# Kernel optimization log

Measured on AMD Instinct MI355X. Metric: run time of the kernel, lower is better.

## Reference

```python
import jax, jax.numpy as jnp
import numpy as np

EMB, HEADS, DEPTH, SEQ, BATCH = 256, 8, 4, 8192, 4
DH = EMB // HEADS  # 32
FF = 4 * EMB
EPS = 1e-5


def setup_inputs() -> dict:
    key = jax.random.key(0)
    ks = jax.random.split(key, 8)
    w = lambda k, shape: jax.random.normal(k, shape, dtype=jnp.float32) * 0.02
    D = DEPTH
    return {
        "x": jax.random.normal(ks[0], (BATCH, SEQ, EMB), dtype=jnp.float32),
        "Wq": w(ks[1], (D, EMB, EMB)),
        "Wk": w(ks[2], (D, EMB, EMB)),
        "Wv": w(ks[3], (D, EMB, EMB)),
        "Wo": w(ks[4], (D, EMB, EMB)),
        "bo": jnp.zeros((D, EMB), jnp.float32),
        "ln1_g": jnp.ones((D, EMB), jnp.float32),
        "ln1_b": jnp.zeros((D, EMB), jnp.float32),
        "W1": w(ks[5], (D, EMB, FF)),
        "b1": jnp.zeros((D, FF), jnp.float32),
        "W2": w(ks[6], (D, FF, EMB)),
        "b2": jnp.zeros((D, EMB), jnp.float32),
        "ln2_g": jnp.ones((D, EMB), jnp.float32),
        "ln2_b": jnp.zeros((D, EMB), jnp.float32),
    }


def _layernorm(x, g, b):
    mu = x.mean(-1, keepdims=True)
    var = ((x - mu) ** 2).mean(-1, keepdims=True)
    return (x - mu) * jax.lax.rsqrt(var + EPS) * g + b


def _linear_attn(x, Wq, Wk, Wv, Wo, bo):
    # lucidrains linear_attn: q,k scaled by d**-0.25; softmax q over feature dim,
    # k over sequence dim; context = k^T v (per head), out = q @ context.
    b, n, dm = x.shape
    split = lambda t: t.reshape(b, n, HEADS, DH).transpose(0, 2, 1, 3)  # -> bhnd
    scale = DH ** -0.25
    q = jax.nn.softmax(split(x @ Wq) * scale, axis=-1)   # over d
    k = jax.nn.softmax(split(x @ Wk) * scale, axis=-2)   # over n
    v = split(x @ Wv)
    context = jnp.einsum('bhnd,bhne->bhde', k, v)        # [b,h,d,d]
    out = jnp.einsum('bhnd,bhde->bhne', q, context)      # [b,h,n,d]
    out = out.transpose(0, 2, 1, 3).reshape(b, n, dm)
    return out @ Wo + bo


def _forward(x, Wq, Wk, Wv, Wo, bo, ln1_g, ln1_b, W1, b1, W2, b2, ln2_g, ln2_b):
    for i in range(DEPTH):
        h = _layernorm(x, ln1_g[i], ln1_b[i])
        x = x + _linear_attn(h, Wq[i], Wk[i], Wv[i], Wo[i], bo[i])
        h = _layernorm(x, ln2_g[i], ln2_b[i])
        x = x + (jax.nn.gelu(h @ W1[i] + b1[i], approximate=False) @ W2[i] + b2[i])
    return x


def reference(x, Wq, Wk, Wv, Wo, bo, ln1_g, ln1_b, W1, b1, W2, b2, ln2_g, ln2_b):
    return _forward(x, Wq, Wk, Wv, Wo, bo, ln1_g, ln1_b, W1, b1, W2, b2, ln2_g, ln2_b)
```

## Files before the change

### kernel.cpp

```cpp
#include <hip/hip_runtime.h>
#include <hip/hip_bf16.h>

typedef __attribute__((ext_vector_type(8))) short bf16x8;
typedef __attribute__((ext_vector_type(4))) float f32x4;

#define EMB 256
#define HEADS 8
#define DH 32
#define SEQ 8192
#define BATCH 4
#define NROWS (SEQ*BATCH)
#define FFD 1024
#define DEPTH 4
#define QKVN 768
#define SCALE 0.42044820762685725f
#define NCHUNK 128
#define ROWS_PER_CHUNK (SEQ/NCHUNK)

static __device__ __forceinline__ float bf2f(ushort u){
  union { unsigned int i; float f; } x; x.i = ((unsigned int)u) << 16; return x.f;
}
static __device__ __forceinline__ ushort f2bf(float f){
  union { __hip_bfloat16 h; ushort u; } cv;
  cv.h = __float2bfloat16(f);
  return cv.u;
}
static __device__ __forceinline__ float gelu_f(float v){
  float y = 0.7978845608028654f * (v + 0.044715f*v*v*v);
  float e = __expf(2.0f*y);
  return 0.5f*v*(1.0f + (1.0f - 2.0f/(e + 1.0f)));
}

static __device__ __forceinline__ void gload_lds16(const ushort* g, ushort* l){
  __builtin_amdgcn_global_load_lds(
      (const __attribute__((address_space(1))) unsigned int*)(uintptr_t)g,
      (__attribute__((address_space(3))) unsigned int*)(uintptr_t)l,
      16, 0, 0);
}

__global__ __launch_bounds__(256) void prep_weights(
    const float* __restrict__ Wq, const float* __restrict__ Wk,
    const float* __restrict__ Wv, const float* __restrict__ Wo,
    const float* __restrict__ W1, const float* __restrict__ W2,
    ushort* __restrict__ wqkv_t, ushort* __restrict__ wo_t,
    ushort* __restrict__ w1_t, ushort* __restrict__ w2_t)
{
  __shared__ float tile[32][33];
  int bid = blockIdx.x;
  int L = bid / 768, r = bid % 768;
  const float* src; ushort* dst; int K, N, tidx;
  if (r < 192){ int which = r >> 6; tidx = r & 63;
    src = (which==0?Wq:which==1?Wk:Wv) + (long)L*65536;
    dst = wqkv_t + (long)L*QKVN*EMB + which*EMB*EMB; K=256; N=256;
  } else if (r < 256){ tidx = r-192; src = Wo + (long)L*65536; dst = wo_t + (long)L*65536; K=256; N=256; }
  else if (r < 512){ tidx = r-256; src = W1 + (long)L*262144; dst = w1_t + (long)L*262144; K=256; N=1024; }
  else { tidx = r-512; src = W2 + (long)L*262144; dst = w2_t + (long)L*262144; K=1024; N=256; }
  int tn = N >> 5;
  int tk = tidx / tn, tj = tidx % tn;
  int k0 = tk*32, n0 = tj*32;
  int c = threadIdx.x & 31, r0 = threadIdx.x >> 5;
  #pragma unroll
  for (int i=0;i<4;i++){
    int rr = r0 + i*8;
    tile[rr][c] = src[(long)(k0+rr)*N + n0 + c];
  }
  __syncthreads();
  #pragma unroll
  for (int i=0;i<4;i++){
    int rr = r0 + i*8;
    dst[(long)(n0+rr)*K + k0 + c] = f2bf(tile[c][rr]);
  }
}

__global__ __launch_bounds__(256) void ln_kernel(const float* __restrict__ x,
    const float* __restrict__ g, const float* __restrict__ bb,
    ushort* __restrict__ h)
{
  int wid = threadIdx.x >> 6, lane = threadIdx.x & 63;
  long row = (long)blockIdx.x*4 + wid;
  const float4 xv = *(const float4*)(x + row*EMB + lane*4);
  float s = xv.x+xv.y+xv.z+xv.w;
  float s2 = xv.x*xv.x+xv.y*xv.y+xv.z*xv.z+xv.w*xv.w;
  #pragma unroll
  for (int m=1;m<64;m<<=1){ s += __shfl_xor(s,m,64); s2 += __shfl_xor(s2,m,64); }
  float mean = s * (1.0f/EMB);
  float inv = rsqrtf(s2*(1.0f/EMB) - mean*mean + 1e-5f);
  float4 gv = *(const float4*)(g + lane*4);
  float4 bv = *(const float4*)(bb + lane*4);
  ushort4 o;
  o.x = f2bf((xv.x-mean)*inv*gv.x + bv.x);
  o.y = f2bf((xv.y-mean)*inv*gv.y + bv.y);
  o.z = f2bf((xv.z-mean)*inv*gv.z + bv.z);
  o.w = f2bf((xv.w-mean)*inv*gv.w + bv.w);
  *(ushort4*)(h + row*EMB + lane*4) = o;
}

template<int MODE, int BM, int BN, int BK, int GSWAP>
__global__ __launch_bounds__(512, 2) void gemm_bt(
    const ushort* __restrict__ A, const ushort* __restrict__ Bt,
    int M, int N, int K,
    const float* __restrict__ bias,
    const float* __restrict__ xinf, const ushort* __restrict__ xinb,
    float* __restrict__ xoutf, ushort* __restrict__ xoutb,
    ushort* __restrict__ outb,
    const float* __restrict__ lng, const float* __restrict__ lnb)
{
  constexpr int NF = BN/64;
  constexpr int MR = BM/32;
  constexpr int MH = MR/4;
  constexpr int KK = BK/32;
  constexpr int CPR = BK/8;
  constexpr int AI = BM*BK/4096;
  constexpr int BI = BN*BK/4096;
  constexpr int TI = AI + BI;
  constexpr int NPH = KK*MH;
  __shared__ ushort LDSraw[2*BM*BK + 2*BN*BK];
  ushort* Abuf0 = LDSraw;
  ushort* Abuf1 = LDSraw + BM*BK;
  ushort* Bbuf0 = LDSraw + 2*BM*BK;
  ushort* Bbuf1 = LDSraw + 2*BM*BK + BN*BK;
  int t = threadIdx.x;
  int lane = t & 63, wid = t >> 6;
  int wr = wid >> 2, wc = wid & 3;
  int wrb = wr*(BM/2), wcb = wc*(BN/4);
  long rowA0, colB0;
  if (GSWAP){ rowA0 = (long)blockIdx.y * BM; colB0 = (long)blockIdx.x * BN; }
  else      { rowA0 = (long)blockIdx.x * BM; colB0 = (long)blockIdx.y * BN; }
  const ushort* gA[AI]; int dA[AI];
  #pragma unroll
  for (int i=0;i<AI;i++){
    int l = i*512 + t;
    int row = l / CPR;
    int clog = (t % CPR) ^ (row & (CPR-1));
    gA[i] = A + (rowA0 + row)*(long)K + clog*8;
    dA[i] = l*8;
  }
  const ushort* gB[BI]; int dB[BI];
  #pragma unroll
  for (int i=0;i<BI;i++){
    int l = i*512 + t;
    int row = l / CPR;
    int clog = (t % CPR) ^ (row & (CPR-1));
    gB[i] = Bt + (colB0 + row)*(long)K + clog*8;
    dB[i] = l*8;
  }
  ushort* Ac = Abuf0; ushort* An = Abuf1;
  ushort* Bc = Bbuf0; ushort* Bn = Bbuf1;
  f32x4 acc[MR][NF] = {};
  int fr = lane & 15, cr4 = lane >> 4;
  int nsteps = K / BK;
  #pragma unroll
  for (int i=0;i<AI;i++) gload_lds16(gA[i], Ac + dA[i]);
  #pragma unroll
  for (int i=0;i<BI;i++) gload_lds16(gB[i], Bc + dB[i]);
  asm volatile("s_waitcnt vmcnt(0)" ::: "memory");
  __syncthreads();
  for (int s = 0; s < nsteps; ++s){
    bool pf = (s+1 < nsteps);
    long knext = (long)(s+1) * BK;
    #pragma unroll
    for (int kk=0; kk<KK; ++kk){
      int chunk = (((kk*4 + cr4)) ^ (fr & (CPR-1))) << 3;
      bf16x8 bv[NF];
      #pragma unroll
      for (int n=0;n<NF;n++)
        bv[n] = *(const bf16x8*)(Bc + (wcb + n*16 + fr)*BK + chunk);
      #pragma unroll
      for (int mh=0; mh<MH; ++mh){
        int sp = kk*MH + mh;
        bf16x8 av[4];
        #pragma unroll
        for (int m=0;m<4;m++)
          av[m] = *(const bf16x8*)(Ac + (wrb + (mh*4+m)*16 + fr)*BK + chunk);
        if (pf){
          #pragma unroll
          for (int j=0;j<TI;j++){
            if (j*NPH >= sp*TI && j*NPH < (sp+1)*TI){
              if (j < AI) gload_lds16(gA[j]+knext, An+dA[j]);
              else        gload_lds16(gB[j-AI]+knext, Bn+dB[j-AI]);
            }
          }
        }
        __builtin_amdgcn_s_setprio(1);
        #pragma unroll
        for (int m=0;m<4;m++){
          #pragma unroll
          for (int n=0;n<NF;n++)
            acc[mh*4+m][n] = __builtin_amdgcn_mfma_f32_16x16x32_bf16(av[m], bv[n], acc[mh*4+m][n], 0,0,0);
        }
        __builtin_amdgcn_s_setprio(0);
      }
    }
    asm volatile("s_waitcnt vmcnt(0)" ::: "memory");
    __syncthreads();
    ushort* tp;
    tp = Ac; Ac = An; An = tp;
    tp = Bc; Bc = Bn; Bn = tp;
  }
  constexpr int BNP = BN + 4;
  constexpr int ROUNDS = BM/32;
  constexpr int RPH = BM/64;
  float* bounce = (float*)LDSraw;
  int fq = lane >> 4;
  constexpr int TPR = BN/4;
  int rdrow = t / TPR;
  int rdcol = (t % TPR) * 4;
  constexpr int RPP = 512 / TPR;
  constexpr int PASSES = 32 / RPP;
  long gcf = colB0 + rdcol;
  float4 bv4e = {0,0,0,0}, g4e = {0,0,0,0}, b4e = {0,0,0,0};
  if (MODE==2 || MODE==3 || MODE==4) bv4e = *(const float4*)&bias[gcf];
  if (MODE==3 || MODE==4){ g4e = *(const float4*)&lng[gcf]; b4e = *(const float4*)&lnb[gcf]; }
  #pragma unroll
  for (int r = 0; r < ROUNDS; ++r){
    __syncthreads();
    if (wr == r / RPH){
      int mb = (r % RPH)*2;
      #pragma unroll
      for (int m4=0;m4<2;m4++){
        #pragma unroll
        for (int n=0;n<NF;n++){
          #pragma unroll
          for (int i=0;i<4;i++)
            bounce[(m4*16 + fq*4 + i)*BNP + wcb + n*16 + fr] = acc[mb+m4][n][i];
        }
      }
    }
    __syncthreads();
    long gr0 = rowA0 + r*32;
    #pragma unroll
    for (int p=0;p<PASSES;p++){
      int lr = p*RPP + rdrow;
      long gr = gr0 + lr;
      float4 v = *(float4*)&bounce[lr*BNP + rdcol];
      if (MODE==0){
        ushort4 o; o.x=f2bf(v.x); o.y=f2bf(v.y); o.z=f2bf(v.z); o.w=f2bf(v.w);
        *(ushort4*)&outb[gr*N + gcf] = o;
      } else if (MODE==2){
        ushort4 o;
        o.x = f2bf(gelu_f(v.x + bv4e.x)); o.y = f2bf(gelu_f(v.y + bv4e.y));
        o.z = f2bf(gelu_f(v.z + bv4e.z)); o.w = f2bf(gelu_f(v.w + bv4e.w));
        *(ushort4*)&outb[gr*N + gcf] = o;
      } else {
        float xo0, xo1, xo2, xo3;
        if (MODE==3){
          const float4 xo = *(const float4*)&xinf[gr*N + gcf];
          xo0=xo.x; xo1=xo.y; xo2=xo.z; xo3=xo.w;
        } else {
          const ushort4 xb = *(const ushort4*)&xinb[gr*N + gcf];
          xo0=bf2f(xb.x); xo1=bf2f(xb.y); xo2=bf2f(xb.z); xo3=bf2f(xb.w);
        }
        v.x += bv4e.x + xo0; v.y += bv4e.y + xo1;
        v.z += bv4e.z + xo2; v.w += bv4e.w + xo3;
        ushort4 xw;
        xw.x=f2bf(v.x); xw.y=f2bf(v.y); xw.z=f2bf(v.z); xw.w=f2bf(v.w);
        *(ushort4*)&xoutb[gr*N + gcf] = xw;
        float s1 = v.x+v.y+v.z+v.w;
        float s2 = v.x*v.x+v.y*v.y+v.z*v.z+v.w*v.w;
        #pragma unroll
        for (int mm=1;mm<64;mm<<=1){ s1 += __shfl_xor(s1,mm,64); s2 += __shfl_xor(s2,mm,64); }
        float mean = s1 * (1.0f/EMB);
        float inv = rsqrtf(s2*(1.0f/EMB) - mean*mean + 1e-5f);
        ushort4 o;
        o.x = f2bf((v.x-mean)*inv*g4e.x + b4e.x);
        o.y = f2bf((v.y-mean)*inv*g4e.y + b4e.y);
        o.z = f2bf((v.z-mean)*inv*g4e.z + b4e.z);
        o.w = f2bf((v.w-mean)*inv*g4e.w + b4e.w);
        *(ushort4*)&outb[gr*EMB + gcf] = o;
      }
    }
  }
}

template<int MODE>
__global__ __launch_bounds__(512) void ff_fused(
    const ushort* __restrict__ A, const ushort* __restrict__ w1t,
    const ushort* __restrict__ w2t,
    const float* __restrict__ b1, const float* __restrict__ b2,
    const ushort* __restrict__ xinb,
    float* __restrict__ xoutf, ushort* __restrict__ xoutb,
    ushort* __restrict__ hout,
    const float* __restrict__ lng, const float* __restrict__ lnb)
{
  __shared__ ushort As[128*256];
  __shared__ ushort W1b[64*256];
  __shared__ ushort W2b[256*64];
  __shared__ ushort Ps[128*68];
  int t = threadIdx.x, lane = t & 63, wid = t >> 6;
  int fr = lane & 15, cr4 = lane >> 4, fq = lane >> 4;
  long rowA0 = (long)blockIdx.x * 128;
  #pragma unroll
  for (int i=0;i<8;i++){
    int l = i*512 + t;
    int row = l >> 5;
    int clog = (l & 31) ^ (row & 31);
    gload_lds16(A + (rowA0+row)*256 + clog*8, As + l*8);
  }
  #pragma unroll
  for (int i=0;i<4;i++){
    int l = i*512 + t;
    int row = l >> 5;
    int clog = (l & 31) ^ (row & 31);
    gload_lds16(w1t + row*256 + clog*8, W1b + l*8);
  }
  asm volatile("s_waitcnt vmcnt(0)" ::: "memory");
  __syncthreads();
  int rwP = (wid & 3)*32, fwP = (wid >> 2)*32;
  int rw2 = (wid >> 2)*64, cw2 = (wid & 3)*64;
  f32x4 accC[4][4] = {};
  for (int j = 0; j < 16; ++j){
    float bvp0 = b1[j*64 + fwP + fr];
    float bvp1 = b1[j*64 + fwP + 16 + fr];
    f32x4 accP[2][2] = {};
    #pragma unroll
    for (int kk=0; kk<8; ++kk){
      if (kk < 4){
        int l = kk*512 + t;
        int row = l >> 3, c = l & 7;
        int clog = c ^ (row & 7);
        gload_lds16(w2t + row*1024 + j*64 + clog*8, W2b + l*8);
      }
      int ci = kk*4 + cr4;
      bf16x8 av[2], wv[2];
      #pragma unroll
      for (int m=0;m<2;m++){
        int row = rwP + m*16 + fr;
        av[m] = *(const bf16x8*)(As + row*256 + ((ci ^ (row&31)) << 3));
      }
      #pragma unroll
      for (int n=0;n<2;n++){
        int row = fwP + n*16 + fr;
        wv[n] = *(const bf16x8*)(W1b + row*256 + ((ci ^ (row&31)) << 3));
      }
      __builtin_amdgcn_s_setprio(1);
      #pragma unroll
      for (int m=0;m<2;m++){
        #pragma unroll
        for (int n=0;n<2;n++)
          accP[m][n] = __builtin_amdgcn_mfma_f32_16x16x32_bf16(av[m], wv[n], accP[m][n], 0,0,0);
      }
      __builtin_amdgcn_s_setprio(0);
    }
    #pragma unroll
    for (int n=0;n<2;n++){
      float bv = (n==0) ? bvp0 : bvp1;
      #pragma unroll
      for (int m=0;m<2;m++){
        #pragma unroll
        for (int i2=0;i2<4;i2++){
          int row = rwP + m*16 + fq*4 + i2;
          Ps[row*68 + fwP + n*16 + fr] = f2bf(gelu_f(accP[m][n][i2] + bv));
        }
      }
    }
    asm volatile("s_waitcnt vmcnt(0)" ::: "memory");
    __syncthreads();
    bool pw1 = (j+1 < 16);
    #pragma unroll
    for (int kk2=0; kk2<2; ++kk2){
      if (pw1 && kk2==0){
        #pragma unroll
        for (int ii=0;ii<4;ii++){
          int l = ii*512 + t;
          int row = l >> 5;
          int clog = (l & 31) ^ (row & 31);
          gload_lds16(w1t + (long)(j+1)*64*256 + row*256 + clog*8, W1b + l*8);
        }
      }
      int ci2 = kk2*4 + cr4;
      bf16x8 pv[4], wv2[4];
      #pragma unroll
      for (int m=0;m<4;m++){
        int row = rw2 + m*16 + fr;
        pv[m] = *(const bf16x8*)(Ps + row*68 + ci2*8);
      }
      #pragma unroll
      for (int n=0;n<4;n++){
        int row = cw2 + n*16 + fr;
        wv2[n] = *(const bf16x8*)(W2b + row*64 + ((ci2 ^ (row&7)) << 3));
      }
      __builtin_amdgcn_s_setprio(1);
      #pragma unroll
      for (int m=0;m<4;m++){
        #pragma unroll
        for (int n=0;n<4;n++)
          accC[m][n] = __builtin_amdgcn_mfma_f32_16x16x32_bf16(pv[m], wv2[n], accC[m][n], 0,0,0);
      }
      __builtin_amdgcn_s_setprio(0);
    }
    asm volatile("s_waitcnt vmcnt(0)" ::: "memory");
    __syncthreads();
  }
  float* bounce = (float*)As;
  int rdrow = t >> 6;
  int rdcol = (t & 63) * 4;
  const float4 bv4 = *(const float4*)&b2[rdcol];
  float4 g4 = {0,0,0,0}, b4 = {0,0,0,0};
  if (MODE==4){ g4 = *(const float4*)&lng[rdcol]; b4 = *(const float4*)&lnb[rdcol]; }
  #pragma unroll
  for (int r = 0; r < 4; ++r){
    __syncthreads();
    if ((wid >> 2) == (r >> 1)){
      int mb = (r & 1)*2;
      #pragma unroll
      for (int m4=0;m4<2;m4++){
        #pragma unroll
        for (int n=0;n<4;n++){
          #pragma unroll
          for (int i2=0;i2<4;i2++)
            bounce[(m4*16 + fq*4 + i2)*260 + cw2 + n*16 + fr] = accC[mb+m4][n][i2];
        }
      }
    }
    __syncthreads();
    long gr0 = rowA0 + r*32;
    #pragma unroll
    for (int p=0;p<4;p++){
      int lr = p*8 + rdrow;
      long gr = gr0 + lr;
      float4 v = *(float4*)&bounce[lr*260 + rdcol];
      const ushort4 xb4 = *(const ushort4*)&xinb[gr*EMB + rdcol];
      v.x += bv4.x + bf2f(xb4.x); v.y += bv4.y + bf2f(xb4.y);
      v.z += bv4.z + bf2f(xb4.z); v.w += bv4.w + bf2f(xb4.w);
      if (MODE==5){
        *(float4*)&xoutf[gr*EMB + rdcol] = v;
      } else {
        ushort4 xw;
        xw.x=f2bf(v.x); xw.y=f2bf(v.y); xw.z=f2bf(v.z); xw.w=f2bf(v.w);
        *(ushort4*)&xoutb[gr*EMB + rdcol] = xw;
        float s1 = v.x+v.y+v.z+v.w;
        float s2 = v.x*v.x+v.y*v.y+v.z*v.z+v.w*v.w;
        #pragma unroll
        for (int mm=1;mm<64;mm<<=1){ s1 += __shfl_xor(s1,mm,64); s2 += __shfl_xor(s2,mm,64); }
        float mean = s1 * (1.0f/EMB);
        float inv = rsqrtf(s2*(1.0f/EMB) - mean*mean + 1e-5f);
        ushort4 o;
        o.x = f2bf((v.x-mean)*inv*g4.x + b4.x);
        o.y = f2bf((v.y-mean)*inv*g4.y + b4.y);
        o.z = f2bf((v.z-mean)*inv*g4.z + b4.z);
        o.w = f2bf((v.w-mean)*inv*g4.w + b4.w);
        *(ushort4*)&hout[gr*EMB + rdcol] = o;
      }
    }
  }
}

__global__ __launch_bounds__(256) void colstats_partial(const ushort* __restrict__ qkv,
    float* __restrict__ pmax, float* __restrict__ psum)
{
  int ch = blockIdx.x, b = blockIdx.y;
  int t = threadIdx.x;
  const ushort* base = qkv + ((long)b*SEQ + (long)ch*ROWS_PER_CHUNK)*QKVN + EMB + t;
  float m[4] = {-1e30f,-1e30f,-1e30f,-1e30f};
  float s[4] = {0.f,0.f,0.f,0.f};
  #pragma unroll 2
  for (int n = 0; n < ROWS_PER_CHUNK; n += 4){
    #pragma unroll
    for (int j=0;j<4;j++){
      float v = bf2f(base[(long)(n+j)*QKVN]) * SCALE;
      float m2 = fmaxf(m[j], v);
      s[j] = s[j]*__expf(m[j]-m2) + __expf(v-m2);
      m[j] = m2;
    }
  }
  float M = fmaxf(fmaxf(m[0],m[1]), fmaxf(m[2],m[3]));
  float S = s[0]*__expf(m[0]-M) + s[1]*__expf(m[1]-M)
          + s[2]*__expf(m[2]-M) + s[3]*__expf(m[3]-M);
  long idx = ((long)b*NCHUNK + ch)*EMB + t;
  pmax[idx] = M; psum[idx] = S;
}

__global__ __launch_bounds__(256) void colstats_reduce(const float* __restrict__ pmax,
    const float* __restrict__ psum, float* __restrict__ kmax, float* __restrict__ ksum)
{
  int b = blockIdx.x, t = threadIdx.x;
  const float* pm = pmax + (long)b*NCHUNK*EMB + t;
  const float* ps = psum + (long)b*NCHUNK*EMB + t;
  float m = -1e30f, s = 0.f;
  for (int c = 0; c < NCHUNK; ++c){
    float cm = pm[(long)c*EMB], cs = ps[(long)c*EMB];
    float m2 = fmaxf(m, cm);
    s = s*__expf(m-m2) + cs*__expf(cm-m2);
    m = m2;
  }
  kmax[b*EMB + t] = m;
  ksum[b*EMB + t] = s;
}

__global__ __launch_bounds__(256) void ctx_partial(
    const ushort* __restrict__ qkv, const float* __restrict__ kmax,
    float* __restrict__ ctx_part)
{
  constexpr int LT = 72;
  __shared__ ushort ekT[32*LT];
  __shared__ ushort vvT[32*LT];
  int ch = blockIdx.x, h = blockIdx.y, b = blockIdx.z;
  int t = threadIdx.x, lane = t & 63, wid = t >> 6;
  long nbase = (long)b*SEQ + ch*512;
  int lrow = t >> 2, lseg = (t & 3) << 3;
  float km[8];
  #pragma unroll
  for (int j=0;j<8;j++) km[j] = kmax[b*256 + h*DH + lseg + j];
  int wstep = wid & 1, wdr = (wid >> 1) << 4;
  f32x4 acc0 = {}, acc1 = {};
  int frow = lane & 15, g8 = (lane >> 4) << 3;
  for (int st = 0; st < 8; ++st){
    long n0 = nbase + st*64;
    const ushort* gk = qkv + (n0 + lrow)*QKVN + EMB + h*DH + lseg;
    uint4 kv = *(const uint4*)gk;
    uint4 vv = *(const uint4*)(gk + EMB);
    __syncthreads();
    const ushort* kp = (const ushort*)&kv;
    const ushort* vp = (const ushort*)&vv;
    #pragma unroll
    for (int j=0;j<8;j++){
      float f = bf2f(kp[j])*SCALE;
      ekT[(lseg+j)*LT + lrow] = f2bf(__expf(f - km[j]));
      vvT[(lseg+j)*LT + lrow] = vp[j];
    }
    __syncthreads();
    bf16x8 afr = *(const bf16x8*)(ekT + (wdr + frow)*LT + wstep*32 + g8);
    bf16x8 bf0 = *(const bf16x8*)(vvT + frow*LT + wstep*32 + g8);
    bf16x8 bf1 = *(const bf16x8*)(vvT + (16 + frow)*LT + wstep*32 + g8);
    acc0 = __builtin_amdgcn_mfma_f32_16x16x32_bf16(afr, bf0, acc0, 0,0,0);
    acc1 = __builtin_amdgcn_mfma_f32_16x16x32_bf16(afr, bf1, acc1, 0,0,0);
  }
  int fq = lane >> 4;
  long pb = (((long)(b*HEADS+h))*32 + (ch*2+wstep))*1024;
  #pragma unroll
  for (int i=0;i<4;i++){
    ctx_part[pb + (wdr + fq*4 + i)*32 + frow] = acc0[i];
    ctx_part[pb + (wdr + fq*4 + i)*32 + 16 + frow] = acc1[i];
  }
}

__global__ __launch_bounds__(256) void ctx_reduce(const float* __restrict__ ctx_part,
    const float* __restrict__ ksum, ushort* __restrict__ ctxT)
{
  int bh = blockIdx.x; int b = bh >> 3, h = bh & 7;
  int t = threadIdx.x; int d = t >> 3, e4 = (t & 7) << 2;
  const float* p = ctx_part + (long)bh*32768 + d*32 + e4;
  float sx=0, sy=0, sz=0, sw=0;
  for (int c=0;c<32;c++){
    const float4 v = *(const float4*)(p + c*1024);
    sx+=v.x; sy+=v.y; sz+=v.z; sw+=v.w;
  }
  float inv = 1.0f / ksum[b*256 + h*DH + d];
  long base = (long)bh*1024;
  ctxT[base + (e4+0)*32 + d] = f2bf(sx*inv);
  ctxT[base + (e4+1)*32 + d] = f2bf(sy*inv);
  ctxT[base + (e4+2)*32 + d] = f2bf(sz*inv);
  ctxT[base + (e4+3)*32 + d] = f2bf(sw*inv);
}

__global__ __launch_bounds__(256) void attn_out(
    const ushort* __restrict__ qkv, const ushort* __restrict__ ctxT,
    ushort* __restrict__ ao)
{
  __shared__ ushort sq[4][16][264];
  int t = threadIdx.x, lane = t & 63, wid = t >> 6;
  long row0 = (long)blockIdx.x*64 + wid*16;
  int b = (int)(row0 / SEQ);
  int fr = lane & 15, g = lane >> 4;
  bf16x8 cf[8][2];
  #pragma unroll
  for (int h=0;h<8;h++){
    #pragma unroll
    for (int eh=0;eh<2;eh++)
      cf[h][eh] = *(const bf16x8*)(ctxT + ((long)(b*8+h)*32 + eh*16 + fr)*32 + g*8);
  }
  long gr = row0 + fr;
  #pragma unroll
  for (int hh=0;hh<2;hh++){
    int h = g*2 + hh;
    const ushort* qp = qkv + gr*QKVN + h*DH;
    union { uint4 v[4]; ushort u[32]; } qq;
    qq.v[0]=*(const uint4*)qp; qq.v[1]=*(const uint4*)(qp+8);
    qq.v[2]=*(const uint4*)(qp+16); qq.v[3]=*(const uint4*)(qp+24);
    float f[32]; float m = -1e30f;
    #pragma unroll
    for (int j=0;j<32;j++){ f[j] = bf2f(qq.u[j])*SCALE; m = fmaxf(m, f[j]); }
    float ssum = 0.f;
    #pragma unroll
    for (int j=0;j<32;j++){ f[j] = __expf(f[j]-m); ssum += f[j]; }
    float inv = 1.0f/ssum;
    union { uint4 v[4]; ushort u[32]; } oo;
    #pragma unroll
    for (int j=0;j<32;j++) oo.u[j] = f2bf(f[j]*inv);
    ushort* dst = &sq[wid][fr][h*DH];
    #pragma unroll
    for (int c2=0;c2<4;c2++) *(uint4*)(dst + c2*8) = oo.v[c2];
  }
  __syncthreads();
  #pragma unroll
  for (int h=0;h<8;h++){
    bf16x8 af = *(const bf16x8*)(&sq[wid][fr][h*DH + g*8]);
    f32x4 z = {};
    f32x4 o0 = __builtin_amdgcn_mfma_f32_16x16x32_bf16(af, cf[h][0], z, 0,0,0);
    f32x4 o1 = __builtin_amdgcn_mfma_f32_16x16x32_bf16(af, cf[h][1], z, 0,0,0);
    #pragma unroll
    for (int i=0;i<4;i++){
      long r = row0 + g*4 + i;
      ao[r*EMB + h*DH + fr]      = f2bf(o0[i]);
      ao[r*EMB + h*DH + 16 + fr] = f2bf(o1[i]);
    }
  }
}

extern "C" void kernel_launch(void* const* d_in, const int* in_sizes, int n_in,
                              void* d_out, int out_size, void* d_ws, size_t ws_size,
                              hipStream_t stream)
{
  const float* x_in = (const float*)d_in[0];
  const float* Wq  = (const float*)d_in[1];
  const float* Wk  = (const float*)d_in[2];
  const float* Wv  = (const float*)d_in[3];
  const float* Wo  = (const float*)d_in[4];
  const float* bo  = (const float*)d_in[5];
  const float* ln1g = (const float*)d_in[6];
  const float* ln1b = (const float*)d_in[7];
  const float* W1  = (const float*)d_in[8];
  const float* b1  = (const float*)d_in[9];
  const float* W2  = (const float*)d_in[10];
  const float* b2  = (const float*)d_in[11];
  const float* ln2g = (const float*)d_in[12];
  const float* ln2b = (const float*)d_in[13];
  float* xout = (float*)d_out;

  char* ws = (char*)d_ws;
  ushort* h_buf  = (ushort*)ws;  ws += (long)NROWS*EMB*2;
  ushort* xb     = (ushort*)ws;  ws += (long)NROWS*EMB*2;
  ushort* big    = (ushort*)ws;  ws += (long)NROWS*FFD*2;
  ushort* wqkv_t = (ushort*)ws;  ws += (long)DEPTH*QKVN*EMB*2;
  ushort* wo_t   = (ushort*)ws;  ws += (long)DEPTH*EMB*EMB*2;
  ushort* w1_t   = (ushort*)ws;  ws += (long)DEPTH*FFD*EMB*2;
  ushort* w2_t   = (ushort*)ws;  ws += (long)DEPTH*EMB*FFD*2;
  float*  kmax   = (float*)ws;   ws += (long)BATCH*EMB*4;
  float*  ksumv  = (float*)ws;   ws += (long)BATCH*EMB*4;
  float*  ctx_part = (float*)ws; ws += (long)BATCH*HEADS*32*1024*4;
  ushort* ctxT   = (ushort*)ws;  ws += (long)BATCH*HEADS*1024*2;
  float*  pmax   = (float*)ws;   ws += (long)BATCH*NCHUNK*EMB*4;
  float*  psum   = (float*)ws;   ws += (long)BATCH*NCHUNK*EMB*4;

  prep_weights<<<3072, 256, 0, stream>>>(Wq, Wk, Wv, Wo, W1, W2, wqkv_t, wo_t, w1_t, w2_t);
  ln_kernel<<<NROWS/4, 256, 0, stream>>>(x_in, ln1g, ln1b, h_buf);

  ushort* qkv = big;
  for (int L = 0; L < DEPTH; ++L){
    gemm_bt<0,128,256,32,1><<<dim3(QKVN/256, NROWS/128), 512, 0, stream>>>(
        h_buf, wqkv_t + (long)L*QKVN*EMB, NROWS, QKVN, EMB,
        nullptr, nullptr, nullptr, nullptr, nullptr, qkv, nullptr, nullptr);
    colstats_partial<<<dim3(NCHUNK, BATCH), 256, 0, stream>>>(qkv, pmax, psum);
    colstats_reduce<<<BATCH, 256, 0, stream>>>(pmax, psum, kmax, ksumv);
    ctx_partial<<<dim3(16, HEADS, BATCH), 256, 0, stream>>>(qkv, kmax, ctx_part);
    ctx_reduce<<<32, 256, 0, stream>>>(ctx_part, ksumv, ctxT);
    attn_out<<<NROWS/64, 256, 0, stream>>>(qkv, ctxT, h_buf);
    if (L == 0){
      gemm_bt<3,128,256,64,0><<<dim3(NROWS/128, 1), 512, 0, stream>>>(
          h_buf, wo_t, NROWS, EMB, EMB,
          bo, x_in, nullptr, nullptr, xb, h_buf, ln2g, ln2b);
    } else {
      gemm_bt<4,128,256,64,0><<<dim3(NROWS/128, 1), 512, 0, stream>>>(
          h_buf, wo_t + (long)L*EMB*EMB, NROWS, EMB, EMB,
          bo + L*EMB, nullptr, xb, nullptr, xb, h_buf,
          ln2g + L*EMB, ln2b + L*EMB);
    }
    if (L + 1 < DEPTH){
      ff_fused<4><<<256, 512, 0, stream>>>(
          h_buf, w1_t + (long)L*FFD*EMB, w2_t + (long)L*EMB*FFD,
          b1 + L*FFD, b2 + L*EMB, xb, nullptr, xb, h_buf,
          ln1g + (L+1)*EMB, ln1b + (L+1)*EMB);
    } else {
      ff_fused<5><<<256, 512, 0, stream>>>(
          h_buf, w1_t + (long)L*FFD*EMB, w2_t + (long)L*EMB*FFD,
          b1 + L*FFD, b2 + L*EMB, xb, xout, nullptr, nullptr,
          nullptr, nullptr);
    }
  }
}
```

Before: 566.7 us.

## Fuse output projection, residual and LayerNorm into the feed-forward kernel

Each 128-row block now runs the Wo projection in a new kernel, streaming Wo in double-buffered 64-column slices. The residual plus LayerNorm2 result is written straight into the swizzled LDS A tile, and the block then continues with the existing fused FF1/GELU/FF2 path. This drops one kernel launch per layer and the global write and re-read of the LN2 activations. In exchange it writes the mid-layer residual to a new xmid buffer, needs a larger LDS footprint (about 148 KB), and lengthens each block.

```diff
diff --git a/kernel.cpp b/kernel.cpp
--- a/kernel.cpp
+++ b/kernel.cpp
@@ -99,11 +99,7 @@
 __global__ __launch_bounds__(512, 2) void gemm_bt(
     const ushort* __restrict__ A, const ushort* __restrict__ Bt,
     int M, int N, int K,
-    const float* __restrict__ bias,
-    const float* __restrict__ xinf, const ushort* __restrict__ xinb,
-    float* __restrict__ xoutf, ushort* __restrict__ xoutb,
-    ushort* __restrict__ outb,
-    const float* __restrict__ lng, const float* __restrict__ lnb)
+    ushort* __restrict__ outb)
 {
   constexpr int NF = BN/64;
   constexpr int MR = BM/32;
@@ -208,9 +204,6 @@
   constexpr int RPP = 512 / TPR;
   constexpr int PASSES = 32 / RPP;
   long gcf = colB0 + rdcol;
-  float4 bv4e = {0,0,0,0}, g4e = {0,0,0,0}, b4e = {0,0,0,0};
-  if (MODE==2 || MODE==3 || MODE==4) bv4e = *(const float4*)&bias[gcf];
-  if (MODE==3 || MODE==4){ g4e = *(const float4*)&lng[gcf]; b4e = *(const float4*)&lnb[gcf]; }
   #pragma unroll
   for (int r = 0; r < ROUNDS; ++r){
     __syncthreads();
@@ -233,75 +226,152 @@
       int lr = p*RPP + rdrow;
       long gr = gr0 + lr;
       float4 v = *(float4*)&bounce[lr*BNP + rdcol];
-      if (MODE==0){
-        ushort4 o; o.x=f2bf(v.x); o.y=f2bf(v.y); o.z=f2bf(v.z); o.w=f2bf(v.w);
-        *(ushort4*)&outb[gr*N + gcf] = o;
-      } else if (MODE==2){
-        ushort4 o;
-        o.x = f2bf(gelu_f(v.x + bv4e.x)); o.y = f2bf(gelu_f(v.y + bv4e.y));
-        o.z = f2bf(gelu_f(v.z + bv4e.z)); o.w = f2bf(gelu_f(v.w + bv4e.w));
-        *(ushort4*)&outb[gr*N + gcf] = o;
-      } else {
-        float xo0, xo1, xo2, xo3;
-        if (MODE==3){
-          const float4 xo = *(const float4*)&xinf[gr*N + gcf];
-          xo0=xo.x; xo1=xo.y; xo2=xo.z; xo3=xo.w;
-        } else {
-          const ushort4 xb = *(const ushort4*)&xinb[gr*N + gcf];
-          xo0=bf2f(xb.x); xo1=bf2f(xb.y); xo2=bf2f(xb.z); xo3=bf2f(xb.w);
-        }
-        v.x += bv4e.x + xo0; v.y += bv4e.y + xo1;
-        v.z += bv4e.z + xo2; v.w += bv4e.w + xo3;
-        ushort4 xw;
-        xw.x=f2bf(v.x); xw.y=f2bf(v.y); xw.z=f2bf(v.z); xw.w=f2bf(v.w);
-        *(ushort4*)&xoutb[gr*N + gcf] = xw;
-        float s1 = v.x+v.y+v.z+v.w;
-        float s2 = v.x*v.x+v.y*v.y+v.z*v.z+v.w*v.w;
-        #pragma unroll
-        for (int mm=1;mm<64;mm<<=1){ s1 += __shfl_xor(s1,mm,64); s2 += __shfl_xor(s2,mm,64); }
-        float mean = s1 * (1.0f/EMB);
-        float inv = rsqrtf(s2*(1.0f/EMB) - mean*mean + 1e-5f);
-        ushort4 o;
-        o.x = f2bf((v.x-mean)*inv*g4e.x + b4e.x);
-        o.y = f2bf((v.y-mean)*inv*g4e.y + b4e.y);
-        o.z = f2bf((v.z-mean)*inv*g4e.z + b4e.z);
-        o.w = f2bf((v.w-mean)*inv*g4e.w + b4e.w);
-        *(ushort4*)&outb[gr*EMB + gcf] = o;
-      }
-    }
-  }
-}
-
-template<int MODE>
-__global__ __launch_bounds__(512) void ff_fused(
-    const ushort* __restrict__ A, const ushort* __restrict__ w1t,
-    const ushort* __restrict__ w2t,
-    const float* __restrict__ b1, const float* __restrict__ b2,
-    const ushort* __restrict__ xinb,
+      ushort4 o; o.x=f2bf(v.x); o.y=f2bf(v.y); o.z=f2bf(v.z); o.w=f2bf(v.w);
+      *(ushort4*)&outb[gr*N + gcf] = o;
+    }
+  }
+}
+
+template<int WMODE, int FMODE>
+__global__ __launch_bounds__(512) void wo_ff_fused(
+    const ushort* __restrict__ aattn, const ushort* __restrict__ wot,
+    const ushort* __restrict__ w1t, const ushort* __restrict__ w2t,
+    const float* __restrict__ bo_, const float* __restrict__ b1,
+    const float* __restrict__ b2,
+    const float* __restrict__ xinf, const ushort* __restrict__ xinb,
+    ushort* __restrict__ xmid,
     float* __restrict__ xoutf, ushort* __restrict__ xoutb,
     ushort* __restrict__ hout,
-    const float* __restrict__ lng, const float* __restrict__ lnb)
-{
-  __shared__ ushort As[128*256];
-  __shared__ ushort W1b[64*256];
-  __shared__ ushort W2b[256*64];
-  __shared__ ushort Ps[128*68];
+    const float* __restrict__ ln2g, const float* __restrict__ ln2b,
+    const float* __restrict__ ln1g_, const float* __restrict__ ln1b_)
+{
+  __shared__ ushort LDS[74240];
+  ushort* As = LDS;
+  ushort* R1 = LDS + 32768;
+  ushort* R2 = LDS + 49152;
+  ushort* Ps = LDS + 65536;
   int t = threadIdx.x, lane = t & 63, wid = t >> 6;
   int fr = lane & 15, cr4 = lane >> 4, fq = lane >> 4;
   long rowA0 = (long)blockIdx.x * 128;
+  int wr = wid >> 2, wc = wid & 3;
+  int wrb = wr*64, wcb = wc*64;
   #pragma unroll
   for (int i=0;i<8;i++){
     int l = i*512 + t;
     int row = l >> 5;
     int clog = (l & 31) ^ (row & 31);
-    gload_lds16(A + (rowA0+row)*256 + clog*8, As + l*8);
+    gload_lds16(aattn + (rowA0+row)*256 + clog*8, As + l*8);
+  }
+  #pragma unroll
+  for (int i=0;i<4;i++){
+    int l = i*512 + t;
+    int row = l >> 3;
+    int clog = (l & 7) ^ (row & 7);
+    gload_lds16(wot + row*256 + clog*8, R1 + l*8);
+  }
+  asm volatile("s_waitcnt vmcnt(0)" ::: "memory");
+  __syncthreads();
+  f32x4 accW[4][4] = {};
+  for (int c = 0; c < 4; ++c){
+    const ushort* Wc = (c&1) ? R2 : R1;
+    ushort* Wn = (c&1) ? R1 : R2;
+    #pragma unroll
+    for (int kk=0; kk<2; ++kk){
+      if (kk==0 && c<3){
+        #pragma unroll
+        for (int i=0;i<4;i++){
+          int l = i*512 + t;
+          int row = l >> 3;
+          int clog = (l & 7) ^ (row & 7);
+          gload_lds16(wot + row*256 + (c+1)*64 + clog*8, Wn + l*8);
+        }
+      }
+      int ci2 = kk*4 + cr4;
+      bf16x8 av[4], bv[4];
+      #pragma unroll
+      for (int m=0;m<4;m++){
+        int row = wrb + m*16 + fr;
+        int gc2 = c*8 + ci2;
+        av[m] = *(const bf16x8*)(As + row*256 + ((gc2 ^ (row&31)) << 3));
+      }
+      #pragma unroll
+      for (int n=0;n<4;n++){
+        int row = wcb + n*16 + fr;
+        bv[n] = *(const bf16x8*)(Wc + row*64 + ((ci2 ^ (row&7)) << 3));
+      }
+      __builtin_amdgcn_s_setprio(1);
+      #pragma unroll
+      for (int m=0;m<4;m++){
+        #pragma unroll
+        for (int n=0;n<4;n++)
+          accW[m][n] = __builtin_amdgcn_mfma_f32_16x16x32_bf16(av[m], bv[n], accW[m][n], 0,0,0);
+      }
+      __builtin_amdgcn_s_setprio(0);
+    }
+    asm volatile("s_waitcnt vmcnt(0)" ::: "memory");
+    __syncthreads();
   }
   #pragma unroll
   for (int i=0;i<4;i++){
     int l = i*512 + t;
     int row = l >> 5;
     int clog = (l & 31) ^ (row & 31);
-    gload_lds16(w1t + row*256 + clog*8, W1b + l*8);
+    gload_lds16(w1t + row*256 + clog*8, R1 + l*8);
+  }
+  {
+    float* wb = (float*)Ps;
+    int rdrow = t >> 6;
+    int rdcol = (t & 63) * 4;
+    const float4 bo4 = *(const float4*)&bo_[rdcol];
+    const float4 g4 = *(const float4*)&ln2g[rdcol];
+    const float4 bb4 = *(const float4*)&ln2b[rdcol];
+    #pragma unroll
+    for (int r = 0; r < 8; ++r){
+      __syncthreads();
+      if (wr == (r >> 2)){
+        int m = r & 3;
+        #pragma unroll
+        for (int n=0;n<4;n++){
+          #pragma unroll
+          for (int i2=0;i2<4;i2++)
+            wb[(fq*4 + i2)*260 + wcb + n*16 + fr] = accW[m][n][i2];
+        }
+      }
+      __syncthreads();
+      #pragma unroll
+      for (int p=0;p<2;p++){
+        int lr = p*8 + rdrow;
+        int row = r*16 + lr;
+        long gr = rowA0 + row;
+        float4 v = *(float4*)&wb[lr*260 + rdcol];
+        float xo0, xo1, xo2, xo3;
+        if (WMODE==3){
+          const float4 xo = *(const float4*)&xinf[gr*EMB + rdcol];
+          xo0=xo.x; xo1=xo.y; xo2=xo.z; xo3=xo.w;
+        } else {
+          const ushort4 xb4 = *(const ushort4*)&xinb[gr*EMB + rdcol];
+          xo0=bf2f(xb4.x); xo1=bf2f(xb4.y); xo2=bf2f(xb4.z); xo3=bf2f(xb4.w);
+        }
+        v.x += bo4.x + xo0; v.y += bo4.y + xo1;
+        v.z += bo4.z + xo2; v.w += bo4.w + xo3;
+        ushort4 xw;
+        xw.x=f2bf(v.x); xw.y=f2bf(v.y); xw.z=f2bf(v.z); xw.w=f2bf(v.w);
+        *(ushort4*)&xmid[gr*EMB + rdcol] = xw;
+        float s1 = v.x+v.y+v.z+v.w;
+        float s2 = v.x*v.x+v.y*v.y+v.z*v.z+v.w*v.w;
+        #pragma unroll
+        for (int mm=1;mm<64;mm<<=1){ s1 += __shfl_xor(s1,mm,64); s2 += __shfl_xor(s2,mm,64); }
+        float mean = s1 * (1.0f/EMB);
+        float inv = rsqrtf(s2*(1.0f/EMB) - mean*mean + 1e-5f);
+        ushort4 hx;
+        hx.x = f2bf((v.x-mean)*inv*g4.x + bb4.x);
+        hx.y = f2bf((v.y-mean)*inv*g4.y + bb4.y);
+        hx.z = f2bf((v.z-mean)*inv*g4.z + bb4.z);
+        hx.w = f2bf((v.w-mean)*inv*g4.w + bb4.w);
+        int phys = (rdcol >> 3) ^ (row & 31);
+        *(ushort4*)&As[row*256 + phys*8 + (rdcol & 7)] = hx;
+      }
+    }
   }
   asm volatile("s_waitcnt vmcnt(0)" ::: "memory");
   __syncthreads();
@@ -318,7 +388,7 @@
         int l = kk*512 + t;
         int row = l >> 3, c = l & 7;
         int clog = c ^ (row & 7);
-        gload_lds16(w2t + row*1024 + j*64 + clog*8, W2b + l*8);
+        gload_lds16(w2t + row*1024 + j*64 + clog*8, R2 + l*8);
       }
       int ci = kk*4 + cr4;
       bf16x8 av[2], wv[2];
@@ -330,7 +400,7 @@
       #pragma unroll
       for (int n=0;n<2;n++){
         int row = fwP + n*16 + fr;
-        wv[n] = *(const bf16x8*)(W1b + row*256 + ((ci ^ (row&31)) << 3));
+        wv[n] = *(const bf16x8*)(R1 + row*256 + ((ci ^ (row&31)) << 3));
       }
       __builtin_amdgcn_s_setprio(1);
       #pragma unroll
@@ -364,7 +434,7 @@
           int l = ii*512 + t;
           int row = l >> 5;
           int clog = (l & 31) ^ (row & 31);
-          gload_lds16(w1t + (long)(j+1)*64*256 + row*256 + clog*8, W1b + l*8);
+          gload_lds16(w1t + (long)(j+1)*16384 + row*256 + clog*8, R1 + l*8);
         }
       }
       int ci2 = kk2*4 + cr4;
@@ -377,7 +447,7 @@
       #pragma unroll
       for (int n=0;n<4;n++){
         int row = cw2 + n*16 + fr;
-        wv2[n] = *(const bf16x8*)(W2b + row*64 + ((ci2 ^ (row&7)) << 3));
+        wv2[n] = *(const bf16x8*)(R2 + row*64 + ((ci2 ^ (row&7)) << 3));
       }
       __builtin_amdgcn_s_setprio(1);
       #pragma unroll
@@ -391,55 +461,57 @@
     asm volatile("s_waitcnt vmcnt(0)" ::: "memory");
     __syncthreads();
   }
-  float* bounce = (float*)As;
-  int rdrow = t >> 6;
-  int rdcol = (t & 63) * 4;
-  const float4 bv4 = *(const float4*)&b2[rdcol];
-  float4 g4 = {0,0,0,0}, b4 = {0,0,0,0};
-  if (MODE==4){ g4 = *(const float4*)&lng[rdcol]; b4 = *(const float4*)&lnb[rdcol]; }
-  #pragma unroll
-  for (int r = 0; r < 4; ++r){
-    __syncthreads();
-    if ((wid >> 2) == (r >> 1)){
-      int mb = (r & 1)*2;
-      #pragma unroll
-      for (int m4=0;m4<2;m4++){
-        #pragma unroll
-        for (int n=0;n<4;n++){
+  {
+    float* bounce = (float*)As;
+    int rdrow = t >> 6;
+    int rdcol = (t & 63) * 4;
+    const float4 bv4 = *(const float4*)&b2[rdcol];
+    float4 g4 = {0,0,0,0}, b4 = {0,0,0,0};
+    if (FMODE==4){ g4 = *(const float4*)&ln1g_[rdcol]; b4 = *(const float4*)&ln1b_[rdcol]; }
+    #pragma unroll
+    for (int r = 0; r < 4; ++r){
+      __syncthreads();
+      if ((wid >> 2) == (r >> 1)){
+        int mb = (r & 1)*2;
+        #pragma unroll
+        for (int m4=0;m4<2;m4++){
           #pragma unroll
-          for (int i2=0;i2<4;i2++)
-            bounce[(m4*16 + fq*4 + i2)*260 + cw2 + n*16 + fr] = accC[mb+m4][n][i2];
-        }
-      }
-    }
-    __syncthreads();
-    long gr0 = rowA0 + r*32;
-    #pragma unroll
-    for (int p=0;p<4;p++){
-      int lr = p*8 + rdrow;
-      long gr = gr0 + lr;
-      float4 v = *(float4*)&bounce[lr*260 + rdcol];
-      const ushort4 xb4 = *(const ushort4*)&xinb[gr*EMB + rdcol];
-      v.x += bv4.x + bf2f(xb4.x); v.y += bv4.y + bf2f(xb4.y);
-      v.z += bv4.z + bf2f(xb4.z); v.w += bv4.w + bf2f(xb4.w);
-      if (MODE==5){
-        *(float4*)&xoutf[gr*EMB + rdcol] = v;
-      } else {
-        ushort4 xw;
-        xw.x=f2bf(v.x); xw.y=f2bf(v.y); xw.z=f2bf(v.z); xw.w=f2bf(v.w);
-        *(ushort4*)&xoutb[gr*EMB + rdcol] = xw;
-        float s1 = v.x+v.y+v.z+v.w;
-        float s2 = v.x*v.x+v.y*v.y+v.z*v.z+v.w*v.w;
-        #pragma unroll
-        for (int mm=1;mm<64;mm<<=1){ s1 += __shfl_xor(s1,mm,64); s2 += __shfl_xor(s2,mm,64); }
-        float mean = s1 * (1.0f/EMB);
-        float inv = rsqrtf(s2*(1.0f/EMB) - mean*mean + 1e-5f);
-        ushort4 o;
-        o.x = f2bf((v.x-mean)*inv*g4.x + b4.x);
-        o.y = f2bf((v.y-mean)*inv*g4.y + b4.y);
-        o.z = f2bf((v.z-mean)*inv*g4.z + b4.z);
-        o.w = f2bf((v.w-mean)*inv*g4.w + b4.w);
-        *(ushort4*)&hout[gr*EMB + rdcol] = o;
+          for (int n=0;n<4;n++){
+            #pragma unroll
+            for (int i2=0;i2<4;i2++)
+              bounce[(m4*16 + fq*4 + i2)*260 + cw2 + n*16 + fr] = accC[mb+m4][n][i2];
+          }
+        }
+      }
+      __syncthreads();
+      long gr0 = rowA0 + r*32;
+      #pragma unroll
+      for (int p=0;p<4;p++){
+        int lr = p*8 + rdrow;
+        long gr = gr0 + lr;
+        float4 v = *(float4*)&bounce[lr*260 + rdcol];
+        const ushort4 xb4 = *(const ushort4*)&xmid[gr*EMB + rdcol];
+        v.x += bv4.x + bf2f(xb4.x); v.y += bv4.y + bf2f(xb4.y);
+        v.z += bv4.z + bf2f(xb4.z); v.w += bv4.w + bf2f(xb4.w);
+        if (FMODE==5){
+          *(float4*)&xoutf[gr*EMB + rdcol] = v;
+        } else {
+          ushort4 xw;
+          xw.x=f2bf(v.x); xw.y=f2bf(v.y); xw.z=f2bf(v.z); xw.w=f2bf(v.w);
+          *(ushort4*)&xoutb[gr*EMB + rdcol] = xw;
+          float s1 = v.x+v.y+v.z+v.w;
+          float s2 = v.x*v.x+v.y*v.y+v.z*v.z+v.w*v.w;
+          #pragma unroll
+          for (int mm=1;mm<64;mm<<=1){ s1 += __shfl_xor(s1,mm,64); s2 += __shfl_xor(s2,mm,64); }
+          float mean = s1 * (1.0f/EMB);
+          float inv = rsqrtf(s2*(1.0f/EMB) - mean*mean + 1e-5f);
+          ushort4 o;
+          o.x = f2bf((v.x-mean)*inv*g4.x + b4.x);
+          o.y = f2bf((v.y-mean)*inv*g4.y + b4.y);
+          o.z = f2bf((v.z-mean)*inv*g4.z + b4.z);
+          o.w = f2bf((v.w-mean)*inv*g4.w + b4.w);
+          *(ushort4*)&hout[gr*EMB + rdcol] = o;
+        }
       }
     }
   }
@@ -630,6 +702,7 @@
   char* ws = (char*)d_ws;
   ushort* h_buf  = (ushort*)ws;  ws += (long)NROWS*EMB*2;
   ushort* xb     = (ushort*)ws;  ws += (long)NROWS*EMB*2;
+  ushort* xmid   = (ushort*)ws;  ws += (long)NROWS*EMB*2;
   ushort* big    = (ushort*)ws;  ws += (long)NROWS*FFD*2;
   ushort* wqkv_t = (ushort*)ws;  ws += (long)DEPTH*QKVN*EMB*2;
   ushort* wo_t   = (ushort*)ws;  ws += (long)DEPTH*EMB*EMB*2;
@@ -648,33 +721,29 @@
   ushort* qkv = big;
   for (int L = 0; L < DEPTH; ++L){
     gemm_bt<0,128,256,32,1><<<dim3(QKVN/256, NROWS/128), 512, 0, stream>>>(
-        h_buf, wqkv_t + (long)L*QKVN*EMB, NROWS, QKVN, EMB,
-        nullptr, nullptr, nullptr, nullptr, nullptr, qkv, nullptr, nullptr);
+        h_buf, wqkv_t + (long)L*QKVN*EMB, NROWS, QKVN, EMB, qkv);
     colstats_partial<<<dim3(NCHUNK, BATCH), 256, 0, stream>>>(qkv, pmax, psum);
     colstats_reduce<<<BATCH, 256, 0, stream>>>(pmax, psum, kmax, ksumv);
     ctx_partial<<<dim3(16, HEADS, BATCH), 256, 0, stream>>>(qkv, kmax, ctx_part);
     ctx_reduce<<<32, 256, 0, stream>>>(ctx_part, ksumv, ctxT);
     attn_out<<<NROWS/64, 256, 0, stream>>>(qkv, ctxT, h_buf);
-    if (L == 0){
-      gemm_bt<3,128,256,64,0><<<dim3(NROWS/128, 1), 512, 0, stream>>>(
-          h_buf, wo_t, NROWS, EMB, EMB,
-          bo, x_in, nullptr, nullptr, xb, h_buf, ln2g, ln2b);
+    if (L == 0 && DEPTH > 1){
+      wo_ff_fused<3,4><<<NROWS/128, 512, 0, stream>>>(
+          h_buf, wo_t, w1_t, w2_t, bo, b1, b2,
+          x_in, nullptr, xmid, nullptr, xb, h_buf,
+          ln2g, ln2b, ln1g + EMB, ln1b + EMB);
+    } else if (L + 1 < DEPTH){
+      wo_ff_fused<4,4><<<NROWS/128, 512, 0, stream>>>(
+          h_buf, wo_t + (long)L*EMB*EMB, w1_t + (long)L*FFD*EMB, w2_t + (long)L*EMB*FFD,
+          bo + L*EMB, b1 + L*FFD, b2 + L*EMB,
+          nullptr, xb, xmid, nullptr, xb, h_buf,
+          ln2g + L*EMB, ln2b + L*EMB, ln1g + (L+1)*EMB, ln1b + (L+1)*EMB);
     } else {
-      gemm_bt<4,128,256,64,0><<<dim3(NROWS/128, 1), 512, 0, stream>>>(
-          h_buf, wo_t + (long)L*EMB*EMB, NROWS, EMB, EMB,
-          bo + L*EMB, nullptr, xb, nullptr, xb, h_buf,
-          ln2g + L*EMB, ln2b + L*EMB);
-    }
-    if (L + 1 < DEPTH){
-      ff_fused<4><<<256, 512, 0, stream>>>(
-          h_buf, w1_t + (long)L*FFD*EMB, w2_t + (long)L*EMB*FFD,
-          b1 + L*FFD, b2 + L*EMB, xb, nullptr, xb, h_buf,
-          ln1g + (L+1)*EMB, ln1b + (L+1)*EMB);
-    } else {
-      ff_fused<5><<<256, 512, 0, stream>>>(
-          h_buf, w1_t + (long)L*FFD*EMB, w2_t + (long)L*EMB*FFD,
-          b1 + L*FFD, b2 + L*EMB, xb, xout, nullptr, nullptr,
-          nullptr, nullptr);
-    }
-  }
-}
+      wo_ff_fused<4,5><<<NROWS/128, 512, 0, stream>>>(
+          h_buf, wo_t + (long)L*EMB*EMB, w1_t + (long)L*FFD*EMB, w2_t + (long)L*EMB*FFD,
+          bo + L*EMB, b1 + L*FFD, b2 + L*EMB,
+          nullptr, xb, xmid, xout, nullptr, nullptr,
+          ln2g + L*EMB, ln2b + L*EMB, nullptr, nullptr);
+    }
+  }
+}
```

New measurement: 635.0 us. 12.0% more time.
